# Kernel tuning notes

Hardware: AMD Instinct MI355X
Metric: run time of the kernel (lower is better)

## Reference

```python
import jax, jax.numpy as jnp
import numpy as np

NUM_HEADS = 32
NUM_KV_HEADS = 8
HEAD_DIM = 128
WINDOW = 256
NUM_META = 128
ROPE_BASE = 10000.0


def _rope_cos_sin(seq_len, dim, dtype):
    inv_freq = 1.0 / (ROPE_BASE ** (jnp.arange(0, dim, 2, dtype=jnp.float32) / dim))
    pos = jnp.arange(seq_len, dtype=jnp.float32)
    freqs = pos[:, None] * inv_freq[None, :]          # [S, dim/2]
    emb = jnp.concatenate([freqs, freqs], axis=-1)     # [S, dim]
    return emb.astype(dtype) * 0 + jnp.cos(emb).astype(dtype), jnp.sin(emb).astype(dtype)


def _rotate_half(x):
    x1, x2 = jnp.split(x, 2, axis=-1)
    return jnp.concatenate([-x2, x1], axis=-1)


def setup_inputs() -> dict:
    key = jax.random.key(0)
    k1, k2, k3 = jax.random.split(key, 3)
    B, S = 1, 2176
    return {
        "query_states": jax.random.normal(k1, (B, S, NUM_HEADS * HEAD_DIM), dtype=jnp.float32),
        "key_states": jax.random.normal(k2, (B, S, NUM_KV_HEADS * HEAD_DIM), dtype=jnp.float32),
        "value_states": jax.random.normal(k3, (B, S, NUM_KV_HEADS * HEAD_DIM), dtype=jnp.float32),
    }


def reference(query_states, key_states, value_states):
    B, S, _ = query_states.shape
    n_rep = NUM_HEADS // NUM_KV_HEADS

    q = query_states.reshape(B, S, NUM_HEADS, HEAD_DIM).transpose(0, 2, 1, 3)      # [B,H,S,D]
    k = key_states.reshape(B, S, NUM_KV_HEADS, HEAD_DIM).transpose(0, 2, 1, 3)     # [B,Hk,S,D]
    v = value_states.reshape(B, S, NUM_KV_HEADS, HEAD_DIM).transpose(0, 2, 1, 3)

    # GQA expansion: repeat_interleave along head dim
    k = jnp.repeat(k, n_rep, axis=1)   # [B,H,S,D]
    v = jnp.repeat(v, n_rep, axis=1)

    # inline RoPE on q and (expanded) k
    cos, sin = _rope_cos_sin(S, HEAD_DIM, q.dtype)     # [S,D]
    cos = cos[None, None]
    sin = sin[None, None]
    q = q * cos + _rotate_half(q) * sin
    k = k * cos + _rotate_half(k) * sin

    scale = 1.0 / jnp.sqrt(jnp.asarray(HEAD_DIM, q.dtype))
    scores = jnp.einsum("bhqd,bhkd->bhqk", q, k) * scale

    # mask: causal AND (sliding window OR kv is a prefix meta token)
    q_idx = jnp.arange(S)[:, None]
    kv_idx = jnp.arange(S)[None, :]
    causal = q_idx >= kv_idx
    sliding = (q_idx - kv_idx) <= WINDOW
    prefix = kv_idx < NUM_META
    mask = causal & (sliding | prefix)                 # [S,S]

    scores = jnp.where(mask[None, None], scores, jnp.asarray(-jnp.inf, scores.dtype))
    probs = jax.nn.softmax(scores, axis=-1)
    out = jnp.einsum("bhqk,bhkd->bhqd", probs, v)      # [B,H,S,D]
    return out.transpose(0, 2, 1, 3).reshape(B, S, NUM_HEADS * HEAD_DIM)
```

## Files before the change

kernel.cpp:

```cpp
#include <hip/hip_runtime.h>

#define HQ 32
#define HKV 8
#define DH 128
#define WIN 256
#define META 128
#define QSCALE 0.1275174324f
#define NFREQ 0.20762050594046f
#define INV2PI 0.15915494309189535f

typedef __attribute__((ext_vector_type(8))) __bf16 bf16x8;
typedef __attribute__((ext_vector_type(4))) float f32x4;
typedef unsigned short u16;
typedef unsigned int u32;

__device__ __forceinline__ u16 f2bf(float f) {
  u32 u = __float_as_uint(f);
  u += 0x7FFFu + ((u >> 16) & 1u);
  return (u16)(u >> 16);
}
__device__ __forceinline__ u32 packbf(float a, float b) {
  u32 ua = __float_as_uint(a); ua += 0x7FFFu + ((ua >> 16) & 1u);
  u32 ub = __float_as_uint(b); ub += 0x7FFFu + ((ub >> 16) & 1u);
  return (ua >> 16) | (ub & 0xFFFF0000u);
}

__device__ __forceinline__ void hw_sincos(float pos, float iv_rev, float* s, float* c) {
  float a = __builtin_amdgcn_fractf(pos * iv_rev);
  *s = __builtin_amdgcn_sinf(a);
  *c = __builtin_amdgcn_cosf(a);
}

__global__ __launch_bounds__(256)
void prep_kv(const float* __restrict__ Kg, const float* __restrict__ Vg,
             u16* __restrict__ Kr, u16* __restrict__ Vt, float2* __restrict__ Tab,
             int S) {
  __shared__ float T[32][132];
  const int hk = blockIdx.x;
  const int s0 = blockIdx.y * 32;
  const int tid = threadIdx.x;
  {
    const int r = tid >> 3, c0 = (tid & 7) * 8;
    const int s = s0 + r;
    const float pos = (float)s;
    const float* src = Kg + ((size_t)s * HKV + hk) * DH;
    u16* dst = Kr + ((size_t)hk * S + s) * DH;
    float x[8], y[8];
    #pragma unroll
    for (int j = 0; j < 8; j += 4) {
      *(float4*)&x[j] = *(const float4*)(src + c0 + j);
      *(float4*)&y[j] = *(const float4*)(src + c0 + 64 + j);
    }
    u16 lo[8], hb[8];
    #pragma unroll
    for (int j = 0; j < 8; ++j) {
      float iv = __builtin_amdgcn_exp2f(-NFREQ * (float)(c0 + j)) * INV2PI;
      float sv, cv; hw_sincos(pos, iv, &sv, &cv);
      if (hk == 0) Tab[(size_t)s * 64 + c0 + j] = make_float2(cv, sv);
      lo[j] = f2bf(x[j] * cv - y[j] * sv);
      hb[j] = f2bf(y[j] * cv + x[j] * sv);
    }
    *(int4*)(dst + c0)      = *(int4*)&lo[0];
    *(int4*)(dst + c0 + 64) = *(int4*)&hb[0];
  }
  {
    const int r = tid >> 3, c = (tid & 7) * 16;
    const float* src = Vg + ((size_t)(s0 + r) * HKV + hk) * DH + c;
    #pragma unroll
    for (int j = 0; j < 16; j += 4) *(float4*)&T[r][c + j] = *(const float4*)(src + j);
  }
  __syncthreads();
  {
    const int d = tid >> 1, hf = (tid & 1) * 16;
    u16 buf[16];
    #pragma unroll
    for (int i = 0; i < 16; ++i) buf[i] = f2bf(T[hf + i][d]);
    u16* dst = Vt + ((size_t)hk * DH + d) * S + s0 + hf;
    *(int4*)(dst)     = *(int4*)&buf[0];
    *(int4*)(dst + 8) = *(int4*)&buf[8];
  }
}

#define LOAD_KV(kv0_) do {                                                   \
    const int4* ks_ = (const int4*)(Kb + (size_t)((kv0_) + kr) * DH + ka4 * 32); \
    fk0 = ks_[0]; fk1 = ks_[1]; fk2 = ks_[2]; fk3 = ks_[3];                  \
    const int4* vs_ = (const int4*)(Vb + (kv0_));                            \
    fv0 = vs_[0]; fv1 = vs_[1]; fv2 = vs_[2]; fv3 = vs_[3];                  \
  } while (0)

#define KSLOT(j_) (smem + kr * 256 + ((((ka4 << 2) + (j_)) ^ (kr & 7)) << 4))
#define VSLOT(j_) (Vbase + vr * 128 + ((((vh << 2) + (j_)) ^ (vr & 7)) << 4))
#define STORE_KV() do {                                                      \
    *(int4*)KSLOT(0) = fk0; *(int4*)KSLOT(1) = fk1;                          \
    *(int4*)KSLOT(2) = fk2; *(int4*)KSLOT(3) = fk3;                          \
    *(int4*)VSLOT(0) = fv0; *(int4*)VSLOT(1) = fv1;                          \
    *(int4*)VSLOT(2) = fv2; *(int4*)VSLOT(3) = fv3;                          \
  } while (0)

__global__ __launch_bounds__(256, 4)
void attn_main(const float* __restrict__ Qg, const u16* __restrict__ Kr,
               const u16* __restrict__ Vt, const float2* __restrict__ Tab,
               float* __restrict__ Og, int S) {
  const int h = blockIdx.x;
  const int nqb = gridDim.y;
  const int q0 = (nqb - 1 - (int)blockIdx.y) * 64;
  const int hk = h >> 2;
  const int tid = threadIdx.x;
  const int lane = tid & 63;
  const int wave = tid >> 6;
  const int qid  = lane & 15;
  const int quad = lane >> 4;
  const int swz  = qid & 7;

  __shared__ __align__(16) char smem[40960];
  char* const Vbase = smem + 16384;
  char* const Pbase = smem + 32768;

  const u16* Kb = Kr + (size_t)hk * S * DH;
  const u16* Vb = Vt + ((size_t)hk * DH + (tid >> 1)) * S + (tid & 1) * 32;
  const int kr = tid >> 2, ka4 = tid & 3;
  const int vr = tid >> 1, vh  = tid & 1;

  int4 fk0, fk1, fk2, fk3, fv0, fv1, fv2, fv3;
  LOAD_KV(0);

  {
    const int r = tid >> 2, a = tid & 3, c0 = a * 16;
    const int s = q0 + r;
    const float* qrow = Qg + ((size_t)s * HQ + h) * DH;
    const float2* tb = Tab + (size_t)s * 64 + c0;
    float x[16], y[16];
    float2 t[16];
    #pragma unroll
    for (int j = 0; j < 16; j += 4) {
      *(float4*)&x[j] = *(const float4*)(qrow + c0 + j);
      *(float4*)&y[j] = *(const float4*)(qrow + c0 + 64 + j);
    }
    #pragma unroll
    for (int j = 0; j < 16; j += 2) *(float4*)&t[j] = *(const float4*)(tb + j);
    u16 lo[16], hb[16];
    #pragma unroll
    for (int j = 0; j < 16; ++j) {
      lo[j] = f2bf((x[j] * t[j].x - y[j] * t[j].y) * QSCALE);
      hb[j] = f2bf((y[j] * t[j].x + x[j] * t[j].y) * QSCALE);
    }
    char* qd = smem + r * 256;
    *(int4*)(qd + (((2 * a)     ^ (r & 7)) << 4)) = *(int4*)&lo[0];
    *(int4*)(qd + (((2 * a + 1) ^ (r & 7)) << 4)) = *(int4*)&lo[8];
    *(int4*)(qd + (((2 * a + 8) ^ (r & 7)) << 4)) = *(int4*)&hb[0];
    *(int4*)(qd + (((2 * a + 9) ^ (r & 7)) << 4)) = *(int4*)&hb[8];
  }
  __syncthreads();
  const int qw0 = q0 + wave * 16;
  const int q   = qw0 + qid;
  bf16x8 qa[4];
  {
    const char* qb = smem + (wave * 16 + qid) * 256;
    #pragma unroll
    for (int c = 0; c < 4; ++c)
      qa[c] = *(const bf16x8*)(qb + ((((c << 2) + quad) ^ swz) << 4));
  }
  __syncthreads();
  STORE_KV();
  __syncthreads();

  int wstart = q0 - WIN; if (wstart < META) wstart = META;
  int nwin = (q0 + 64 - wstart) >> 6; if (nwin < 0) nwin = 0;
  const int ntiles = 2 + nwin;

  f32x4 acc[8];
  #pragma unroll
  for (int D = 0; D < 8; ++D)
    #pragma unroll
    for (int r = 0; r < 4; ++r) acc[D][r] = 0.f;
  float m_i = -1e30f, l_i = 0.f;

  for (int t = 0; t < ntiles; ++t) {
    const int kv0 = (t < 2) ? t * 64 : wstart + (t - 2) * 64;
    const bool haveNext = (t + 1 < ntiles);
    if (haveNext) {
      const int kvn = (t + 1 < 2) ? (t + 1) * 64 : wstart + (t - 1) * 64;
      LOAD_KV(kvn);
    }

    const bool active = (kv0 <= qw0 + 15) &&
                        ((kv0 < META) || (qw0 - kv0 - 63 <= WIN));
    if (active) {
      f32x4 sv[4];
      #pragma unroll
      for (int T = 0; T < 4; ++T)
        #pragma unroll
        for (int r = 0; r < 4; ++r) sv[T][r] = 0.f;
      #pragma unroll
      for (int T = 0; T < 4; ++T) {
        const char* ka = smem + (16 * T + qid) * 256;
        #pragma unroll
        for (int c = 0; c < 4; ++c)
          sv[T] = __builtin_amdgcn_mfma_f32_16x16x32_bf16(
                    *(const bf16x8*)(ka + ((((c << 2) + quad) ^ swz) << 4)),
                    qa[c], sv[T], 0, 0, 0);
      }

      const bool fullv = (kv0 + 63 <= qw0) &&
                         ((kv0 + 63 < META) || (qw0 + 15 - kv0 <= WIN));
      if (!fullv) {
        #pragma unroll
        for (int T = 0; T < 4; ++T) {
          #pragma unroll
          for (int r = 0; r < 4; ++r) {
            const int kv = kv0 + 16 * T + 4 * quad + r;
            if (!((kv <= q) && (((q - kv) <= WIN) || (kv < META)))) sv[T][r] = -1e30f;
          }
        }
      }

      float mx = -1e30f;
      #pragma unroll
      for (int T = 0; T < 4; ++T)
        #pragma unroll
        for (int r = 0; r < 4; ++r) mx = fmaxf(mx, sv[T][r]);
      mx = fmaxf(mx, __shfl_xor(mx, 16));
      mx = fmaxf(mx, __shfl_xor(mx, 32));
      if (!__all(mx - m_i <= 8.0f)) {
        const float mnew = fmaxf(m_i, mx);
        const float al = __builtin_amdgcn_exp2f(m_i - mnew);
        m_i = mnew;
        l_i *= al;
        #pragma unroll
        for (int D = 0; D < 8; ++D)
          #pragma unroll
          for (int r = 0; r < 4; ++r) acc[D][r] *= al;
      }
      float ps = 0.f;
      #pragma unroll
      for (int T = 0; T < 4; ++T)
        #pragma unroll
        for (int r = 0; r < 4; ++r) {
          sv[T][r] = __builtin_amdgcn_exp2f(sv[T][r] - m_i);
          ps += sv[T][r];
        }
      l_i += ps;

      {
        char* pw = Pbase + (wave * 16 + qid) * 128;
        #pragma unroll
        for (int T = 0; T < 4; ++T) {
          int2 pr;
          pr.x = (int)packbf(sv[T][0], sv[T][1]);
          pr.y = (int)packbf(sv[T][2], sv[T][3]);
          *(int2*)(pw + ((((T << 1) + (quad >> 1)) ^ swz) << 4) + ((quad & 1) << 3)) = pr;
        }
      }
      const char* pb = Pbase + (wave * 16 + qid) * 128;
      const bf16x8 p0 = *(const bf16x8*)(pb + ((quad ^ swz) << 4));
      const bf16x8 p1 = *(const bf16x8*)(pb + (((4 + quad) ^ swz) << 4));

      #pragma unroll
      for (int D = 0; D < 8; ++D) {
        const char* va = Vbase + (16 * D + qid) * 128;
        acc[D] = __builtin_amdgcn_mfma_f32_16x16x32_bf16(
                   *(const bf16x8*)(va + ((quad ^ swz) << 4)),       p0, acc[D], 0, 0, 0);
        acc[D] = __builtin_amdgcn_mfma_f32_16x16x32_bf16(
                   *(const bf16x8*)(va + (((4 + quad) ^ swz) << 4)), p1, acc[D], 0, 0, 0);
      }
    }

    if (haveNext) {
      __syncthreads();
      STORE_KV();
      __syncthreads();
    }
  }

  l_i += __shfl_xor(l_i, 16);
  l_i += __shfl_xor(l_i, 32);
  const float inv = 1.0f / l_i;
  float* ob = Og + ((size_t)q * HQ + h) * DH;
  #pragma unroll
  for (int D = 0; D < 8; ++D) {
    float4 o = { acc[D][0] * inv, acc[D][1] * inv, acc[D][2] * inv, acc[D][3] * inv };
    *(float4*)(ob + 16 * D + 4 * quad) = o;
  }
}

extern "C" void kernel_launch(void* const* d_in, const int* in_sizes, int n_in,
                              void* d_out, int out_size, void* d_ws, size_t ws_size,
                              hipStream_t stream) {
  const float* Qg = (const float*)d_in[0];
  const float* Kg = (const float*)d_in[1];
  const float* Vg = (const float*)d_in[2];
  float* Og = (float*)d_out;
  const int S = in_sizes[0] / (HQ * DH);

  u16* Kr = (u16*)d_ws;
  u16* Vt = (u16*)((char*)d_ws + (size_t)HKV * S * DH * 2);
  float2* Tab = (float2*)((char*)d_ws + (size_t)HKV * S * DH * 4);

  prep_kv<<<dim3(HKV, S / 32), dim3(256), 0, stream>>>(Kg, Vg, Kr, Vt, Tab, S);
  attn_main<<<dim3(HQ, S / 64), dim3(256), 0, stream>>>(Qg, Kr, Vt, Tab, Og, S);
}
```

Measured before the change: 148.8 us.

## Shrink KV tile from 64 to 32 keys and halve shared memory

Reduces the per-iteration KV tile from 64 to 32 keys, halving LDS use (to 20KB) and the register prefetch buffers, and drops the min-blocks launch bound. The smaller tile gives finer-grained masking and skipping at window edges and allows higher occupancy, but doubles the number of loop iterations and barrier pairs. The V shared-memory layout and P staging are remapped so one MFMA per D block covers 32 keys.

```diff
diff --git a/kernel.cpp b/kernel.cpp
--- a/kernel.cpp
+++ b/kernel.cpp
@@ -81,23 +81,21 @@
   }
 }
 
-#define LOAD_KV(kv0_) do {                                                   \
-    const int4* ks_ = (const int4*)(Kb + (size_t)((kv0_) + kr) * DH + ka4 * 32); \
-    fk0 = ks_[0]; fk1 = ks_[1]; fk2 = ks_[2]; fk3 = ks_[3];                  \
-    const int4* vs_ = (const int4*)(Vb + (kv0_));                            \
-    fv0 = vs_[0]; fv1 = vs_[1]; fv2 = vs_[2]; fv3 = vs_[3];                  \
+#define LOAD_KV(kv0_) do {                                                    \
+    const int4* ks_ = (const int4*)(Kb + (size_t)((kv0_) + kr) * DH + a8 * 16); \
+    fk0 = ks_[0]; fk1 = ks_[1];                                               \
+    const int4* vs_ = (const int4*)(Vbs + (kv0_));                            \
+    fv0 = vs_[0]; fv1 = vs_[1];                                               \
   } while (0)
 
-#define KSLOT(j_) (smem + kr * 256 + ((((ka4 << 2) + (j_)) ^ (kr & 7)) << 4))
-#define VSLOT(j_) (Vbase + vr * 128 + ((((vh << 2) + (j_)) ^ (vr & 7)) << 4))
-#define STORE_KV() do {                                                      \
-    *(int4*)KSLOT(0) = fk0; *(int4*)KSLOT(1) = fk1;                          \
-    *(int4*)KSLOT(2) = fk2; *(int4*)KSLOT(3) = fk3;                          \
-    *(int4*)VSLOT(0) = fv0; *(int4*)VSLOT(1) = fv1;                          \
-    *(int4*)VSLOT(2) = fv2; *(int4*)VSLOT(3) = fv3;                          \
+#define KSLOT(j_) (Kre + kr * 256 + ((((a8 << 1) | (j_)) ^ (kr & 7)) << 4))
+#define VSLOT(j_) (Vre + vr * 128 + ((((q4 << 1) | (j_)) ^ (vr & 7)) << 4))
+#define STORE_KV() do {                                                       \
+    *(int4*)KSLOT(0) = fk0; *(int4*)KSLOT(1) = fk1;                           \
+    *(int4*)VSLOT(0) = fv0; *(int4*)VSLOT(1) = fv1;                           \
   } while (0)
 
-__global__ __launch_bounds__(256, 4)
+__global__ __launch_bounds__(256)
 void attn_main(const float* __restrict__ Qg, const u16* __restrict__ Kr,
                const u16* __restrict__ Vt, const float2* __restrict__ Tab,
                float* __restrict__ Og, int S) {
@@ -112,16 +110,17 @@
   const int quad = lane >> 4;
   const int swz  = qid & 7;
 
-  __shared__ __align__(16) char smem[40960];
-  char* const Vbase = smem + 16384;
-  char* const Pbase = smem + 32768;
+  __shared__ __align__(16) char smem[20480];
+  char* const Kre = smem;
+  char* const Vre = smem + 8192;
+  char* const Pba = smem + 16384;
 
   const u16* Kb = Kr + (size_t)hk * S * DH;
-  const u16* Vb = Vt + ((size_t)hk * DH + (tid >> 1)) * S + (tid & 1) * 32;
-  const int kr = tid >> 2, ka4 = tid & 3;
-  const int vr = tid >> 1, vh  = tid & 1;
-
-  int4 fk0, fk1, fk2, fk3, fv0, fv1, fv2, fv3;
+  const int kr = tid >> 3, a8 = tid & 7;
+  const int vr = tid >> 2, q4 = tid & 3;
+  const u16* Vbs = Vt + ((size_t)hk * DH + (vr + ((q4 >> 1) << 6))) * S + ((q4 & 1) << 4);
+
+  int4 fk0, fk1, fv0, fv1;
   LOAD_KV(0);
 
   {
@@ -164,9 +163,11 @@
   STORE_KV();
   __syncthreads();
 
+  const int mt0 = (q0 + 64) >> 5;
+  const int mt = mt0 < 4 ? mt0 : 4;
   int wstart = q0 - WIN; if (wstart < META) wstart = META;
-  int nwin = (q0 + 64 - wstart) >> 6; if (nwin < 0) nwin = 0;
-  const int ntiles = 2 + nwin;
+  int nwin = (q0 + 64 - wstart) >> 5; if (nwin < 0) nwin = 0;
+  const int ntiles = mt + nwin;
 
   f32x4 acc[8];
   #pragma unroll
@@ -175,25 +176,28 @@
     for (int r = 0; r < 4; ++r) acc[D][r] = 0.f;
   float m_i = -1e30f, l_i = 0.f;
 
+  const int rp = qid & 7, hq = qid >> 3;
+  char* const Pw = Pba + wave * 1024;
+
   for (int t = 0; t < ntiles; ++t) {
-    const int kv0 = (t < 2) ? t * 64 : wstart + (t - 2) * 64;
+    const int kv0 = (t < mt) ? t * 32 : wstart + (t - mt) * 32;
     const bool haveNext = (t + 1 < ntiles);
     if (haveNext) {
-      const int kvn = (t + 1 < 2) ? (t + 1) * 64 : wstart + (t - 1) * 64;
+      const int kvn = (t + 1 < mt) ? (t + 1) * 32 : wstart + (t + 1 - mt) * 32;
       LOAD_KV(kvn);
     }
 
     const bool active = (kv0 <= qw0 + 15) &&
-                        ((kv0 < META) || (qw0 - kv0 - 63 <= WIN));
+                        ((kv0 < META) || (qw0 - kv0 - 31 <= WIN));
     if (active) {
-      f32x4 sv[4];
-      #pragma unroll
-      for (int T = 0; T < 4; ++T)
+      f32x4 sv[2];
+      #pragma unroll
+      for (int T = 0; T < 2; ++T)
         #pragma unroll
         for (int r = 0; r < 4; ++r) sv[T][r] = 0.f;
       #pragma unroll
-      for (int T = 0; T < 4; ++T) {
-        const char* ka = smem + (16 * T + qid) * 256;
+      for (int T = 0; T < 2; ++T) {
+        const char* ka = Kre + (16 * T + qid) * 256;
         #pragma unroll
         for (int c = 0; c < 4; ++c)
           sv[T] = __builtin_amdgcn_mfma_f32_16x16x32_bf16(
@@ -201,11 +205,11 @@
                     qa[c], sv[T], 0, 0, 0);
       }
 
-      const bool fullv = (kv0 + 63 <= qw0) &&
-                         ((kv0 + 63 < META) || (qw0 + 15 - kv0 <= WIN));
+      const bool fullv = (kv0 + 31 <= qw0) &&
+                         ((kv0 + 31 < META) || (qw0 + 15 - kv0 <= WIN));
       if (!fullv) {
         #pragma unroll
-        for (int T = 0; T < 4; ++T) {
+        for (int T = 0; T < 2; ++T) {
           #pragma unroll
           for (int r = 0; r < 4; ++r) {
             const int kv = kv0 + 16 * T + 4 * quad + r;
@@ -216,7 +220,7 @@
 
       float mx = -1e30f;
       #pragma unroll
-      for (int T = 0; T < 4; ++T)
+      for (int T = 0; T < 2; ++T)
         #pragma unroll
         for (int r = 0; r < 4; ++r) mx = fmaxf(mx, sv[T][r]);
       mx = fmaxf(mx, __shfl_xor(mx, 16));
@@ -233,7 +237,7 @@
       }
       float ps = 0.f;
       #pragma unroll
-      for (int T = 0; T < 4; ++T)
+      for (int T = 0; T < 2; ++T)
         #pragma unroll
         for (int r = 0; r < 4; ++r) {
           sv[T][r] = __builtin_amdgcn_exp2f(sv[T][r] - m_i);
@@ -241,27 +245,21 @@
         }
       l_i += ps;
 
-      {
-        char* pw = Pbase + (wave * 16 + qid) * 128;
-        #pragma unroll
-        for (int T = 0; T < 4; ++T) {
-          int2 pr;
-          pr.x = (int)packbf(sv[T][0], sv[T][1]);
-          pr.y = (int)packbf(sv[T][2], sv[T][3]);
-          *(int2*)(pw + ((((T << 1) + (quad >> 1)) ^ swz) << 4) + ((quad & 1) << 3)) = pr;
-        }
-      }
-      const char* pb = Pbase + (wave * 16 + qid) * 128;
-      const bf16x8 p0 = *(const bf16x8*)(pb + ((quad ^ swz) << 4));
-      const bf16x8 p1 = *(const bf16x8*)(pb + (((4 + quad) ^ swz) << 4));
+      #pragma unroll
+      for (int T = 0; T < 2; ++T) {
+        int2 pr;
+        pr.x = (int)packbf(sv[T][0], sv[T][1]);
+        pr.y = (int)packbf(sv[T][2], sv[T][3]);
+        *(int2*)(Pw + rp * 128 + ((((hq << 2) + (T << 1) + (quad >> 1)) ^ rp) << 4)
+                 + ((quad & 1) << 3)) = pr;
+      }
+      const bf16x8 p0 = *(const bf16x8*)(Pw + rp * 128 + ((((hq << 2) + quad) ^ rp) << 4));
 
       #pragma unroll
       for (int D = 0; D < 8; ++D) {
-        const char* va = Vbase + (16 * D + qid) * 128;
-        acc[D] = __builtin_amdgcn_mfma_f32_16x16x32_bf16(
-                   *(const bf16x8*)(va + ((quad ^ swz) << 4)),       p0, acc[D], 0, 0, 0);
-        acc[D] = __builtin_amdgcn_mfma_f32_16x16x32_bf16(
-                   *(const bf16x8*)(va + (((4 + quad) ^ swz) << 4)), p1, acc[D], 0, 0, 0);
+        const char* va = Vre + (16 * (D & 3) + qid) * 128
+                       + (((((D >> 2) << 2) + quad) ^ swz) << 4);
+        acc[D] = __builtin_amdgcn_mfma_f32_16x16x32_bf16(*(const bf16x8*)va, p0, acc[D], 0, 0, 0);
       }
     }
 
```

New measurement: 144.9 us. -2.6%, faster.
